# Optimization experiments

Hardware: AMD Instinct MI355X
Metric: run time of the kernel (lower is better)

Reference implementation:

```python
import jax, jax.numpy as jnp
import numpy as np

N_NODES = 50000
N_EDGES = 1600000
N_FEAT = 256
HIDDEN = 32
N_CLASS = 64
PROP_RANGE = 4
ALPHA = 0.5
BETA = 1.0


def _spmm(edge_src, edge_dst, edge_val, X):
    # sparse propMatrix @ X : gather source rows, scale by edge weight, scatter-add to dst
    msgs = X[edge_src] * edge_val[:, None]            # [E, C]
    return jax.ops.segment_sum(msgs, edge_dst, num_segments=N_NODES)  # [N, C]


def setup_inputs() -> dict:
    key = jax.random.key(0)
    ks = jax.random.split(key, 8)
    x = jax.random.normal(ks[0], (N_NODES, N_FEAT), dtype=jnp.float32)
    edge_src = jax.random.randint(ks[1], (N_EDGES,), 0, N_NODES, dtype=jnp.int32)
    edge_dst = jax.random.randint(ks[2], (N_EDGES,), 0, N_NODES, dtype=jnp.int32)
    edge_val = jax.random.uniform(ks[3], (N_EDGES,), dtype=jnp.float32)
    # predSeq params: Linear(nFeature,32) -> ReLU -> Linear(32,nClass)
    W1 = jax.random.normal(ks[4], (N_FEAT, HIDDEN), dtype=jnp.float32) / np.sqrt(N_FEAT)
    b1 = jnp.zeros((HIDDEN,), dtype=jnp.float32)
    W2 = jax.random.normal(ks[5], (HIDDEN, N_CLASS), dtype=jnp.float32) / np.sqrt(HIDDEN)
    b2 = jnp.zeros((N_CLASS,), dtype=jnp.float32)
    return {"x": x, "edge_src": edge_src, "edge_dst": edge_dst, "edge_val": edge_val,
            "W1": W1, "b1": b1, "W2": W2, "b2": b2}


def reference(x, edge_src, edge_dst, edge_val, W1, b1, W2, b2):
    # predSeq + softmax -> initial pseudo labels [N, nClass]
    h = jax.nn.relu(x @ W1 + b1)
    p = jax.nn.softmax(h @ W2 + b2, axis=1)
    # prop(), mode='none': propRange steps of nonlinear SpMM (dropout = identity in eval)
    for _ in range(PROP_RANGE):
        p = ALPHA * jnp.tanh(BETA * _spmm(edge_src, edge_dst, edge_val, p))
    return jax.nn.softmax(p, axis=1)
```

## Files before the change

kernel.cpp:

```cpp
#include <hip/hip_runtime.h>
#include <hip/hip_bf16.h>
#include <math.h>

#define N_NODES 50000
#define N_EDGES 1600000
#define N_FEAT  256
#define HIDDEN  32
#define N_CLASS 64
#define NBUCK   391
#define EPB     2560
#define BINB    625
#define MLPB    782
#define SCAP    5120
#define CAP     4608

typedef _Float16 half_t;
typedef _Float16 half8 __attribute__((ext_vector_type(8)));

__device__ __forceinline__ float half_tanh(float x) {
  float e = __expf(2.f * x);
  return 0.5f - __builtin_amdgcn_rcpf(e + 1.f);
}


__global__ __launch_bounds__(256) void prep_kernel(
    const float* __restrict__ x, const float* __restrict__ W1,
    const float* __restrict__ b1, const float* __restrict__ W2,
    const float* __restrict__ b2, half_t* __restrict__ P,
    const int* __restrict__ esrc, const int* __restrict__ edst,
    const float* __restrict__ evl, int* __restrict__ bcur,
    int2* __restrict__ st) {
  __shared__ __align__(16) int smem[6684];
  int t = threadIdx.x;

  if (blockIdx.x < MLPB) {
    float* fs = (float*)smem;
    float* xs = fs;
    float* ps = fs;
    float* hfull = fs + 4416;
    int w = __builtin_amdgcn_readfirstlane(t >> 6);
    int l = t & 63;
    int n0 = blockIdx.x * 64;
    int rowb = t >> 4, c4 = t & 15;
    int f0 = c4 * 4;

    float4 v[4];
#pragma unroll
    for (int p = 0; p < 4; ++p) {
      int row = rowb + 16 * p;
      v[p] = make_float4(0.f, 0.f, 0.f, 0.f);
      if (n0 + row < N_NODES)
        v[p] = *(const float4*)(x + (size_t)(n0 + row) * N_FEAT + f0);
    }

    float h[8];
#pragma unroll
    for (int j = 0; j < 8; ++j) h[j] = 0.f;

    for (int kc = 0; kc < 4; ++kc) {
#pragma unroll
      for (int p = 0; p < 4; ++p) {
        int row = rowb + 16 * p;
        int col = (row + f0) & 63;
        xs[(f0 + 0) * 64 + col] = v[p].x;
        xs[(f0 + 1) * 64 + col] = v[p].y;
        xs[(f0 + 2) * 64 + col] = v[p].z;
        xs[(f0 + 3) * 64 + col] = v[p].w;
      }
      __syncthreads();
      if (kc < 3) {
#pragma unroll
        for (int p = 0; p < 4; ++p) {
          int row = rowb + 16 * p;
          v[p] = make_float4(0.f, 0.f, 0.f, 0.f);
          if (n0 + row < N_NODES)
            v[p] = *(const float4*)(x + (size_t)(n0 + row) * N_FEAT + (kc + 1) * 64 + f0);
        }
      }
#pragma unroll 8
      for (int k = 0; k < 64; ++k) {
        float xk = xs[k * 64 + ((l + (k & 60)) & 63)];
        const float* wr = W1 + (size_t)(kc * 64 + k) * HIDDEN + 8 * w;
#pragma unroll
        for (int j = 0; j < 8; ++j) h[j] = fmaf(xk, wr[j], h[j]);
      }
      __syncthreads();
    }

#pragma unroll
    for (int i = 0; i < 8; ++i)
      hfull[l * 33 + 8 * w + i] = fmaxf(h[i] + b1[8 * w + i], 0.f);
    __syncthreads();

    float pa[16];
#pragma unroll
    for (int c = 0; c < 16; ++c) pa[c] = b2[16 * w + c];
#pragma unroll 4
    for (int kk = 0; kk < 32; ++kk) {
      float hk = hfull[l * 33 + kk];
      const float* w2r = W2 + kk * N_CLASS + 16 * w;
#pragma unroll
      for (int c = 0; c < 16; ++c) pa[c] = fmaf(hk, w2r[c], pa[c]);
    }
#pragma unroll
    for (int c = 0; c < 16; ++c) ps[l * 65 + 16 * w + c] = pa[c];
    __syncthreads();

    {
      int n = t >> 2, ck = (t & 3) * 16;
      float q[16];
      float m = -1e30f;
#pragma unroll
      for (int i = 0; i < 16; ++i) { q[i] = ps[n * 65 + ck + i]; m = fmaxf(m, q[i]); }
      m = fmaxf(m, __shfl_xor(m, 1));
      m = fmaxf(m, __shfl_xor(m, 2));
      float s = 0.f;
#pragma unroll
      for (int i = 0; i < 16; ++i) { q[i] = __expf(q[i] - m); s += q[i]; }
      s += __shfl_xor(s, 1);
      s += __shfl_xor(s, 2);
      float inv = 1.f / s;
      if (n0 + n < N_NODES) {
        half8 o0, o1;
#pragma unroll
        for (int i = 0; i < 8; ++i) {
          o0[i] = (half_t)(q[i] * inv);
          o1[i] = (half_t)(q[8 + i] * inv);
        }
        half_t* op = P + (size_t)(n0 + n) * N_CLASS + ck;
        *(half8*)op = o0;
        *(half8*)(op + 8) = o1;
      }
    }
  } else {
    int2* stage = (int2*)smem;
    int* h      = smem + 5120;
    int* lstart = smem + 5511;
    int* lcur   = smem + 5902;
    int* gbase  = smem + 6293;
    int bb = blockIdx.x - MLPB;
    for (int i = t; i < NBUCK; i += 256) { h[i] = 0; lcur[i] = 0; }
    __syncthreads();
    int base = bb * EPB;
    int nloc = min(EPB, N_EDGES - base);
    for (int i = t; i < nloc; i += 256) atomicAdd(&h[edst[base + i] >> 7], 1);
    __syncthreads();
    if (t < 64) {
      int loc[7];
      int s0 = 0;
#pragma unroll
      for (int i = 0; i < 7; ++i) {
        int b = t * 7 + i;
        int c = (b < NBUCK) ? h[b] : 0;
        loc[i] = s0; s0 += c;
      }
      int run = s0;
#pragma unroll
      for (int off = 1; off < 64; off <<= 1) {
        int u = __shfl_up(run, off);
        if (t >= off) run += u;
      }
      int excl = run - s0;
#pragma unroll
      for (int i = 0; i < 7; ++i) {
        int b = t * 7 + i;
        if (b < NBUCK) lstart[b] = excl + loc[i];
      }
    }
    __syncthreads();
    for (int i = t; i < NBUCK; i += 256) {
      int c = h[i];
      gbase[i] = c ? atomicAdd(&bcur[i], c) : 0;
    }
    __syncthreads();
    for (int i = t; i < nloc; i += 256) {
      int e = base + i;
      int d = edst[e];
      int b = d >> 7;
      int pos = lstart[b] + atomicAdd(&lcur[b], 1);
      stage[pos] = make_int2((d << 16) | esrc[e], __float_as_int(evl[e]));
    }
    __syncthreads();
    for (int i = t; i < nloc; i += 256) {
      int2 vv = stage[i];
      int b = (int)(((unsigned)vv.x) >> 23);
      int pos = gbase[b] + (i - lstart[b]);
      if (pos < SCAP) st[(size_t)b * SCAP + pos] = vv;
    }
  }
}


__global__ __launch_bounds__(1024) void build_csr(const int* __restrict__ bcur,
                                                  const int2* __restrict__ st,
                                                  int2* __restrict__ rr,
                                                  int2* __restrict__ ep) {
  __shared__ int2 stage[CAP];
  __shared__ int lh[128], lstart[128], lcur[128];
  int b = blockIdx.x, t = threadIdx.x;
  int n = min(min(bcur[b], SCAP), CAP);
  int gb = b * SCAP;
  if (t < 128) { lh[t] = 0; lcur[t] = 0; }
  __syncthreads();
  for (int i = t; i < n; i += 1024) {
    int2 v = st[gb + i];
    stage[i] = v;
    atomicAdd(&lh[(v.x >> 16) & 127], 1);
  }
  __syncthreads();
  if (t < 64) {
    int a0 = lh[2 * t], a1 = lh[2 * t + 1];
    int s0 = a0 + a1;
    int run = s0;
#pragma unroll
    for (int off = 1; off < 64; off <<= 1) {
      int u = __shfl_up(run, off);
      if (t >= off) run += u;
    }
    int excl = run - s0;
    lstart[2 * t] = excl;
    lstart[2 * t + 1] = excl + a0;
  }
  __syncthreads();
  int nodebase = b * 128;
  int nn = min(128, N_NODES - nodebase);
  if (t < nn)
    rr[nodebase + t] = make_int2(gb + lstart[t], gb + lstart[t] + lh[t]);
  for (int i = t; i < n; i += 1024) {
    int2 v = stage[i];
    int d = (v.x >> 16) & 127;
    int pos = lstart[d] + atomicAdd(&lcur[d], 1);
    ep[gb + pos] = make_int2(v.x & 0xffff, v.y);
  }
}


template <int FINAL>
__global__ __launch_bounds__(256) void spmm_kernel(const int2* __restrict__ rr,
                                                   const long long* __restrict__ epl,
                                                   const half_t* __restrict__ pin,
                                                   void* __restrict__ pout_) {
  int node = blockIdx.x * 4 + (threadIdx.x >> 6);
  int lane = threadIdx.x & 63;
  int g = lane >> 3;
  int s = lane & 7;
  int2 be = rr[node];
  int beg = be.x, end = be.y;
  int deg = end - beg;
  float acc[8];
#pragma unroll
  for (int i = 0; i < 8; ++i) acc[i] = 0.f;
  if (deg <= 64) {
    int idx = beg + lane;
    long long raw = (lane < deg) ? epl[idx] : 0LL;
    int ex = (int)raw;
    float ev = __int_as_float((int)(raw >> 32));
#pragma unroll 4
    for (int j = g; j < deg; j += 8) {
      int   sj = __shfl(ex, j);
      float vj = __shfl(ev, j);
      half8 hv = *(const half8*)(pin + ((size_t)sj << 6) + (s << 3));
#pragma unroll
      for (int i = 0; i < 8; ++i) acc[i] = fmaf(vj, (float)hv[i], acc[i]);
    }
  } else {
    for (int base = beg; base < end; base += 64) {
      int idx = base + lane;
      long long raw = (idx < end) ? epl[idx] : 0LL;
      int ex = (int)raw;
      float ev = __int_as_float((int)(raw >> 32));
      int cnt = min(64, end - base);
#pragma unroll 4
      for (int j = g; j < cnt; j += 8) {
        int   sj = __shfl(ex, j);
        float vj = __shfl(ev, j);
        half8 hv = *(const half8*)(pin + ((size_t)sj << 6) + (s << 3));
#pragma unroll
        for (int i = 0; i < 8; ++i) acc[i] = fmaf(vj, (float)hv[i], acc[i]);
      }
    }
  }
#pragma unroll
  for (int off = 8; off <= 32; off <<= 1)
#pragma unroll
    for (int i = 0; i < 8; ++i) acc[i] += __shfl_xor(acc[i], off);
  float r[8];
#pragma unroll
  for (int i = 0; i < 8; ++i) r[i] = half_tanh(acc[i]);
  if (FINAL) {
    float m = r[0];
#pragma unroll
    for (int i = 1; i < 8; ++i) m = fmaxf(m, r[i]);
    m = fmaxf(m, __shfl_xor(m, 1));
    m = fmaxf(m, __shfl_xor(m, 2));
    m = fmaxf(m, __shfl_xor(m, 4));
    float e[8], sum = 0.f;
#pragma unroll
    for (int i = 0; i < 8; ++i) { e[i] = __expf(r[i] - m); sum += e[i]; }
    sum += __shfl_xor(sum, 1);
    sum += __shfl_xor(sum, 2);
    sum += __shfl_xor(sum, 4);
    float inv = 1.f / sum;
    if (g == 0) {
      float* op = (float*)pout_ + ((size_t)node << 6) + (s << 3);
      *(float4*)op = make_float4(e[0] * inv, e[1] * inv, e[2] * inv, e[3] * inv);
      *(float4*)(op + 4) = make_float4(e[4] * inv, e[5] * inv, e[6] * inv, e[7] * inv);
    }
  } else {
    if (g == 0) {
      half8 o;
#pragma unroll
      for (int i = 0; i < 8; ++i) o[i] = (half_t)r[i];
      *(half8*)((half_t*)pout_ + ((size_t)node << 6) + (s << 3)) = o;
    }
  }
}


extern "C" void kernel_launch(void* const* d_in, const int* in_sizes, int n_in,
                              void* d_out, int out_size, void* d_ws, size_t ws_size,
                              hipStream_t stream) {
  const float* x    = (const float*)d_in[0];
  const int*   esrc = (const int*)d_in[1];
  const int*   edst = (const int*)d_in[2];
  const float* evl  = (const float*)d_in[3];
  const float* W1   = (const float*)d_in[4];
  const float* b1   = (const float*)d_in[5];
  const float* W2   = (const float*)d_in[6];
  const float* b2   = (const float*)d_in[7];

  char* ws = (char*)d_ws;
  int2*   st   = (int2*)  (ws);
  half_t* Pb   = (half_t*)(ws);
  int2*   ep   = (int2*)  (ws + 16015360);
  half_t* Pa   = (half_t*)(ws + 32030720);
  int*    bcur = (int*)   (ws + 38430720);
  int2*   rr   = (int2*)  (ws + 38432320);

  hipMemsetAsync(bcur, 0, NBUCK * sizeof(int), stream);

  prep_kernel<<<MLPB + BINB, 256, 0, stream>>>(x, W1, b1, W2, b2, Pa,
                                               esrc, edst, evl, bcur, st);
  build_csr<<<NBUCK, 1024, 0, stream>>>(bcur, st, rr, ep);

  const long long* epl = (const long long*)ep;
  spmm_kernel<0><<<12500, 256, 0, stream>>>(rr, epl, Pa, (void*)Pb);
  spmm_kernel<0><<<12500, 256, 0, stream>>>(rr, epl, Pb, (void*)Pa);
  spmm_kernel<0><<<12500, 256, 0, stream>>>(rr, epl, Pa, (void*)Pb);
  spmm_kernel<1><<<12500, 256, 0, stream>>>(rr, epl, Pb, d_out);
}
```

Baseline: 267.1 us.

## Fuse CSR build and four SpMM steps into one persistent kernel

Merges build_csr and the four spmm launches into a single kernel of 391 blocks of 1024 threads. Each block keeps its bucket's sorted edge list in shared memory and processes its own 128 destination nodes across all steps, with a hand-written global atomic barrier between steps. This removes launch gaps, the global CSR write, and the edge-list re-reads. In exchange, the SpMM work runs on only 391 blocks (one wave per node), so there is less parallelism and latency hiding. The spin barrier also relies on all blocks being resident at the same time.

```diff
diff --git a/kernel.cpp b/kernel.cpp
--- a/kernel.cpp
+++ b/kernel.cpp
@@ -191,10 +191,28 @@
 }
 
 
-__global__ __launch_bounds__(1024) void build_csr(const int* __restrict__ bcur,
-                                                  const int2* __restrict__ st,
-                                                  int2* __restrict__ rr,
-                                                  int2* __restrict__ ep) {
+__device__ __forceinline__ void gsync(unsigned* __restrict__ bar, int phase) {
+  __syncthreads();
+  if (threadIdx.x == 0) {
+    __threadfence();
+    unsigned old = atomicAdd(&bar[phase], 1u);
+    if (old == NBUCK - 1) {
+      __hip_atomic_store(&bar[4 + phase], 1u, __ATOMIC_RELEASE,
+                         __HIP_MEMORY_SCOPE_AGENT);
+    } else {
+      while (__hip_atomic_load(&bar[4 + phase], __ATOMIC_ACQUIRE,
+                               __HIP_MEMORY_SCOPE_AGENT) == 0)
+        __builtin_amdgcn_s_sleep(8);
+    }
+    __threadfence();
+  }
+  __syncthreads();
+}
+
+__global__ __launch_bounds__(1024, 4) void mega_spmm(
+    const int* __restrict__ bcur, const int2* __restrict__ st,
+    half_t* __restrict__ Pa, half_t* __restrict__ Pb,
+    float* __restrict__ outp, unsigned* __restrict__ bar) {
   __shared__ int2 stage[CAP];
   __shared__ int lh[128], lstart[128], lcur[128];
   int b = blockIdx.x, t = threadIdx.x;
@@ -203,9 +221,9 @@
   if (t < 128) { lh[t] = 0; lcur[t] = 0; }
   __syncthreads();
   for (int i = t; i < n; i += 1024) {
-    int2 v = st[gb + i];
-    stage[i] = v;
-    atomicAdd(&lh[(v.x >> 16) & 127], 1);
+    int2 e = st[gb + i];
+    stage[i] = e;
+    atomicAdd(&lh[(e.x >> 16) & 127], 1);
   }
   __syncthreads();
   if (t < 64) {
@@ -222,97 +240,78 @@
     lstart[2 * t + 1] = excl + a0;
   }
   __syncthreads();
-  int nodebase = b * 128;
-  int nn = min(128, N_NODES - nodebase);
-  if (t < nn)
-    rr[nodebase + t] = make_int2(gb + lstart[t], gb + lstart[t] + lh[t]);
+  int2 v[5]; int pos[5]; int np = 0;
   for (int i = t; i < n; i += 1024) {
-    int2 v = stage[i];
-    int d = (v.x >> 16) & 127;
-    int pos = lstart[d] + atomicAdd(&lcur[d], 1);
-    ep[gb + pos] = make_int2(v.x & 0xffff, v.y);
-  }
-}
-
-
-template <int FINAL>
-__global__ __launch_bounds__(256) void spmm_kernel(const int2* __restrict__ rr,
-                                                   const long long* __restrict__ epl,
-                                                   const half_t* __restrict__ pin,
-                                                   void* __restrict__ pout_) {
-  int node = blockIdx.x * 4 + (threadIdx.x >> 6);
-  int lane = threadIdx.x & 63;
+    int2 e = stage[i];
+    int d = (e.x >> 16) & 127;
+    v[np] = e;
+    pos[np] = lstart[d] + atomicAdd(&lcur[d], 1);
+    ++np;
+  }
+  __syncthreads();
+  for (int k = 0; k < np; ++k) stage[pos[k]] = v[k];
+  __syncthreads();
+
+  int w = t >> 6;
+  int lane = t & 63;
   int g = lane >> 3;
   int s = lane & 7;
-  int2 be = rr[node];
-  int beg = be.x, end = be.y;
-  int deg = end - beg;
-  float acc[8];
-#pragma unroll
-  for (int i = 0; i < 8; ++i) acc[i] = 0.f;
-  if (deg <= 64) {
-    int idx = beg + lane;
-    long long raw = (lane < deg) ? epl[idx] : 0LL;
-    int ex = (int)raw;
-    float ev = __int_as_float((int)(raw >> 32));
+  for (int r = 0; r < 4; ++r) {
+    const half_t* pin = (r & 1) ? Pb : Pa;
+    half_t* pout = (r & 1) ? Pa : Pb;
+#pragma unroll 1
+    for (int ni = 0; ni < 8; ++ni) {
+      int d = w * 8 + ni;
+      int deg = lh[d], base = lstart[d];
+      int node = b * 128 + d;
+      float acc[8];
+#pragma unroll
+      for (int i = 0; i < 8; ++i) acc[i] = 0.f;
 #pragma unroll 4
-    for (int j = g; j < deg; j += 8) {
-      int   sj = __shfl(ex, j);
-      float vj = __shfl(ev, j);
-      half8 hv = *(const half8*)(pin + ((size_t)sj << 6) + (s << 3));
-#pragma unroll
-      for (int i = 0; i < 8; ++i) acc[i] = fmaf(vj, (float)hv[i], acc[i]);
-    }
-  } else {
-    for (int base = beg; base < end; base += 64) {
-      int idx = base + lane;
-      long long raw = (idx < end) ? epl[idx] : 0LL;
-      int ex = (int)raw;
-      float ev = __int_as_float((int)(raw >> 32));
-      int cnt = min(64, end - base);
-#pragma unroll 4
-      for (int j = g; j < cnt; j += 8) {
-        int   sj = __shfl(ex, j);
-        float vj = __shfl(ev, j);
-        half8 hv = *(const half8*)(pin + ((size_t)sj << 6) + (s << 3));
+      for (int j = g; j < deg; j += 8) {
+        int2 e = stage[base + j];
+        float vj = __int_as_float(e.y);
+        int src = e.x & 0xffff;
+        half8 hv = *(const half8*)(pin + ((size_t)src << 6) + (s << 3));
 #pragma unroll
         for (int i = 0; i < 8; ++i) acc[i] = fmaf(vj, (float)hv[i], acc[i]);
       }
-    }
-  }
-#pragma unroll
-  for (int off = 8; off <= 32; off <<= 1)
-#pragma unroll
-    for (int i = 0; i < 8; ++i) acc[i] += __shfl_xor(acc[i], off);
-  float r[8];
-#pragma unroll
-  for (int i = 0; i < 8; ++i) r[i] = half_tanh(acc[i]);
-  if (FINAL) {
-    float m = r[0];
-#pragma unroll
-    for (int i = 1; i < 8; ++i) m = fmaxf(m, r[i]);
-    m = fmaxf(m, __shfl_xor(m, 1));
-    m = fmaxf(m, __shfl_xor(m, 2));
-    m = fmaxf(m, __shfl_xor(m, 4));
-    float e[8], sum = 0.f;
-#pragma unroll
-    for (int i = 0; i < 8; ++i) { e[i] = __expf(r[i] - m); sum += e[i]; }
-    sum += __shfl_xor(sum, 1);
-    sum += __shfl_xor(sum, 2);
-    sum += __shfl_xor(sum, 4);
-    float inv = 1.f / sum;
-    if (g == 0) {
-      float* op = (float*)pout_ + ((size_t)node << 6) + (s << 3);
-      *(float4*)op = make_float4(e[0] * inv, e[1] * inv, e[2] * inv, e[3] * inv);
-      *(float4*)(op + 4) = make_float4(e[4] * inv, e[5] * inv, e[6] * inv, e[7] * inv);
-    }
-  } else {
-    if (g == 0) {
-      half8 o;
-#pragma unroll
-      for (int i = 0; i < 8; ++i) o[i] = (half_t)r[i];
-      *(half8*)((half_t*)pout_ + ((size_t)node << 6) + (s << 3)) = o;
-    }
+#pragma unroll
+      for (int off = 8; off <= 32; off <<= 1)
+#pragma unroll
+        for (int i = 0; i < 8; ++i) acc[i] += __shfl_xor(acc[i], off);
+      float rv[8];
+#pragma unroll
+      for (int i = 0; i < 8; ++i) rv[i] = half_tanh(acc[i]);
+      if (r < 3) {
+        if (g == 0 && node < N_NODES) {
+          half8 o;
+#pragma unroll
+          for (int i = 0; i < 8; ++i) o[i] = (half_t)rv[i];
+          *(half8*)(pout + ((size_t)node << 6) + (s << 3)) = o;
+        }
+      } else {
+        float m = rv[0];
+#pragma unroll
+        for (int i = 1; i < 8; ++i) m = fmaxf(m, rv[i]);
+        m = fmaxf(m, __shfl_xor(m, 1));
+        m = fmaxf(m, __shfl_xor(m, 2));
+        m = fmaxf(m, __shfl_xor(m, 4));
+        float e[8], sum = 0.f;
+#pragma unroll
+        for (int i = 0; i < 8; ++i) { e[i] = __expf(rv[i] - m); sum += e[i]; }
+        sum += __shfl_xor(sum, 1);
+        sum += __shfl_xor(sum, 2);
+        sum += __shfl_xor(sum, 4);
+        float inv = 1.f / sum;
+        if (g == 0 && node < N_NODES) {
+          float* op = outp + ((size_t)node << 6) + (s << 3);
+          *(float4*)op = make_float4(e[0] * inv, e[1] * inv, e[2] * inv, e[3] * inv);
+          *(float4*)(op + 4) = make_float4(e[4] * inv, e[5] * inv, e[6] * inv, e[7] * inv);
+        }
+      }
+    }
+    if (r < 3) gsync(bar, r);
   }
 }
 
@@ -330,22 +329,15 @@
   const float* b2   = (const float*)d_in[7];
 
   char* ws = (char*)d_ws;
-  int2*   st   = (int2*)  (ws);
-  half_t* Pb   = (half_t*)(ws);
-  int2*   ep   = (int2*)  (ws + 16015360);
-  half_t* Pa   = (half_t*)(ws + 32030720);
-  int*    bcur = (int*)   (ws + 38430720);
-  int2*   rr   = (int2*)  (ws + 38432320);
-
-  hipMemsetAsync(bcur, 0, NBUCK * sizeof(int), stream);
+  int2*     st   = (int2*)    (ws);
+  half_t*   Pa   = (half_t*)  (ws + 16015360);
+  half_t*   Pb   = (half_t*)  (ws + 22415360);
+  int*      bcur = (int*)     (ws + 28815360);
+  unsigned* bar  = (unsigned*)(ws + 28816960);
+
+  hipMemsetAsync(ws + 28815360, 0, 1632, stream);
 
   prep_kernel<<<MLPB + BINB, 256, 0, stream>>>(x, W1, b1, W2, b2, Pa,
                                                esrc, edst, evl, bcur, st);
-  build_csr<<<NBUCK, 1024, 0, stream>>>(bcur, st, rr, ep);
-
-  const long long* epl = (const long long*)ep;
-  spmm_kernel<0><<<12500, 256, 0, stream>>>(rr, epl, Pa, (void*)Pb);
-  spmm_kernel<0><<<12500, 256, 0, stream>>>(rr, epl, Pb, (void*)Pa);
-  spmm_kernel<0><<<12500, 256, 0, stream>>>(rr, epl, Pa, (void*)Pb);
-  spmm_kernel<1><<<12500, 256, 0, stream>>>(rr, epl, Pb, d_out);
-}
+  mega_spmm<<<NBUCK, 1024, 0, stream>>>(bcur, st, Pa, Pb, (float*)d_out, bar);
+}
```

After: 528.5 us. 97.9% more time.

## Split propagation feature matrix into two 32-column halves for cache locality

Applied to the files above, without the earlier changes.

Stores the fp16 label matrix as two separate 32-column planes (lo/hi) and runs the three intermediate SpMM steps as a kernel whose blocks each handle one half for a node group. The blocks are interleaved so that each XCD group works on one half. This shrinks the working set each gather touches, aiming for better L2/MALL hit rates on the random source-row reads. Edge list loads become nontemporal. The cost is that every edge list is read twice, once per half, and the blocks are smaller.

```diff
diff --git a/kernel.cpp b/kernel.cpp
--- a/kernel.cpp
+++ b/kernel.cpp
@@ -13,6 +13,7 @@
 #define MLPB    782
 #define SCAP    5120
 #define CAP     4608
+#define SPLITB  25000
 
 typedef _Float16 half_t;
 typedef _Float16 half8 __attribute__((ext_vector_type(8)));
@@ -26,7 +27,8 @@
 __global__ __launch_bounds__(256) void prep_kernel(
     const float* __restrict__ x, const float* __restrict__ W1,
     const float* __restrict__ b1, const float* __restrict__ W2,
-    const float* __restrict__ b2, half_t* __restrict__ P,
+    const float* __restrict__ b2, half_t* __restrict__ Plo,
+    half_t* __restrict__ Phi,
     const int* __restrict__ esrc, const int* __restrict__ edst,
     const float* __restrict__ evl, int* __restrict__ bcur,
     int2* __restrict__ st) {
@@ -127,7 +129,9 @@
           o0[i] = (half_t)(q[i] * inv);
           o1[i] = (half_t)(q[8 + i] * inv);
         }
-        half_t* op = P + (size_t)(n0 + n) * N_CLASS + ck;
+        half_t* op = (ck < 32)
+            ? Plo + (size_t)(n0 + n) * 32 + ck
+            : Phi + (size_t)(n0 + n) * 32 + (ck - 32);
         *(half8*)op = o0;
         *(half8*)(op + 8) = o1;
       }
@@ -235,15 +239,80 @@
 }
 
 
-template <int FINAL>
-__global__ __launch_bounds__(256) void spmm_kernel(const int2* __restrict__ rr,
-                                                   const long long* __restrict__ epl,
-                                                   const half_t* __restrict__ pin,
-                                                   void* __restrict__ pout_) {
+__global__ __launch_bounds__(256) void spmm_half(const int2* __restrict__ rr,
+                                                 const long long* __restrict__ epl,
+                                                 const half_t* __restrict__ plo,
+                                                 const half_t* __restrict__ phi,
+                                                 half_t* __restrict__ qlo,
+                                                 half_t* __restrict__ qhi) {
+  int bid = blockIdx.x;
+  int xc = bid & 7;
+  int hf = xc >> 2;
+  int ng = (bid >> 3) * 4 + (xc & 3);
+  int node = ng * 4 + (threadIdx.x >> 6);
+  int lane = threadIdx.x & 63;
+  int g = lane >> 2;
+  int s = lane & 3;
+  const half_t* pin = hf ? phi : plo;
+  half_t* pout = hf ? qhi : qlo;
+  int2 be = rr[node];
+  int beg = be.x, end = be.y;
+  int deg = end - beg;
+  float acc[8];
+#pragma unroll
+  for (int i = 0; i < 8; ++i) acc[i] = 0.f;
+  if (deg <= 64) {
+    long long raw = (lane < deg) ? __builtin_nontemporal_load(epl + beg + lane) : 0LL;
+    int ex = (int)raw;
+    float ev = __int_as_float((int)(raw >> 32));
+#pragma unroll 4
+    for (int j = g; j < deg; j += 16) {
+      int   sj = __shfl(ex, j);
+      float vj = __shfl(ev, j);
+      half8 hv = *(const half8*)(pin + ((size_t)sj << 5) + (s << 3));
+#pragma unroll
+      for (int i = 0; i < 8; ++i) acc[i] = fmaf(vj, (float)hv[i], acc[i]);
+    }
+  } else {
+    for (int base = beg; base < end; base += 64) {
+      int idx = base + lane;
+      long long raw = (idx < end) ? __builtin_nontemporal_load(epl + idx) : 0LL;
+      int ex = (int)raw;
+      float ev = __int_as_float((int)(raw >> 32));
+      int cnt = min(64, end - base);
+#pragma unroll 4
+      for (int j = g; j < cnt; j += 16) {
+        int   sj = __shfl(ex, j);
+        float vj = __shfl(ev, j);
+        half8 hv = *(const half8*)(pin + ((size_t)sj << 5) + (s << 3));
+#pragma unroll
+        for (int i = 0; i < 8; ++i) acc[i] = fmaf(vj, (float)hv[i], acc[i]);
+      }
+    }
+  }
+#pragma unroll
+  for (int off = 4; off <= 32; off <<= 1)
+#pragma unroll
+    for (int i = 0; i < 8; ++i) acc[i] += __shfl_xor(acc[i], off);
+  if (g == 0) {
+    half8 o;
+#pragma unroll
+    for (int i = 0; i < 8; ++i) o[i] = (half_t)half_tanh(acc[i]);
+    *(half8*)(pout + ((size_t)node << 5) + (s << 3)) = o;
+  }
+}
+
+
+__global__ __launch_bounds__(256) void spmm_final(const int2* __restrict__ rr,
+                                                  const long long* __restrict__ epl,
+                                                  const half_t* __restrict__ plo,
+                                                  const half_t* __restrict__ phi,
+                                                  float* __restrict__ outp) {
   int node = blockIdx.x * 4 + (threadIdx.x >> 6);
   int lane = threadIdx.x & 63;
   int g = lane >> 3;
   int s = lane & 7;
+  const half_t* gb = (s < 4) ? (plo + ((size_t)s << 3)) : (phi + ((size_t)(s - 4) << 3));
   int2 be = rr[node];
   int beg = be.x, end = be.y;
   int deg = end - beg;
@@ -251,22 +320,21 @@
 #pragma unroll
   for (int i = 0; i < 8; ++i) acc[i] = 0.f;
   if (deg <= 64) {
-    int idx = beg + lane;
-    long long raw = (lane < deg) ? epl[idx] : 0LL;
+    long long raw = (lane < deg) ? __builtin_nontemporal_load(epl + beg + lane) : 0LL;
     int ex = (int)raw;
     float ev = __int_as_float((int)(raw >> 32));
 #pragma unroll 4
     for (int j = g; j < deg; j += 8) {
       int   sj = __shfl(ex, j);
       float vj = __shfl(ev, j);
-      half8 hv = *(const half8*)(pin + ((size_t)sj << 6) + (s << 3));
+      half8 hv = *(const half8*)(gb + ((size_t)sj << 5));
 #pragma unroll
       for (int i = 0; i < 8; ++i) acc[i] = fmaf(vj, (float)hv[i], acc[i]);
     }
   } else {
     for (int base = beg; base < end; base += 64) {
       int idx = base + lane;
-      long long raw = (idx < end) ? epl[idx] : 0LL;
+      long long raw = (idx < end) ? __builtin_nontemporal_load(epl + idx) : 0LL;
       int ex = (int)raw;
       float ev = __int_as_float((int)(raw >> 32));
       int cnt = min(64, end - base);
@@ -274,7 +342,7 @@
       for (int j = g; j < cnt; j += 8) {
         int   sj = __shfl(ex, j);
         float vj = __shfl(ev, j);
-        half8 hv = *(const half8*)(pin + ((size_t)sj << 6) + (s << 3));
+        half8 hv = *(const half8*)(gb + ((size_t)sj << 5));
 #pragma unroll
         for (int i = 0; i < 8; ++i) acc[i] = fmaf(vj, (float)hv[i], acc[i]);
       }
@@ -287,32 +355,23 @@
   float r[8];
 #pragma unroll
   for (int i = 0; i < 8; ++i) r[i] = half_tanh(acc[i]);
-  if (FINAL) {
-    float m = r[0];
-#pragma unroll
-    for (int i = 1; i < 8; ++i) m = fmaxf(m, r[i]);
-    m = fmaxf(m, __shfl_xor(m, 1));
-    m = fmaxf(m, __shfl_xor(m, 2));
-    m = fmaxf(m, __shfl_xor(m, 4));
-    float e[8], sum = 0.f;
-#pragma unroll
-    for (int i = 0; i < 8; ++i) { e[i] = __expf(r[i] - m); sum += e[i]; }
-    sum += __shfl_xor(sum, 1);
-    sum += __shfl_xor(sum, 2);
-    sum += __shfl_xor(sum, 4);
-    float inv = 1.f / sum;
-    if (g == 0) {
-      float* op = (float*)pout_ + ((size_t)node << 6) + (s << 3);
-      *(float4*)op = make_float4(e[0] * inv, e[1] * inv, e[2] * inv, e[3] * inv);
-      *(float4*)(op + 4) = make_float4(e[4] * inv, e[5] * inv, e[6] * inv, e[7] * inv);
-    }
-  } else {
-    if (g == 0) {
-      half8 o;
-#pragma unroll
-      for (int i = 0; i < 8; ++i) o[i] = (half_t)r[i];
-      *(half8*)((half_t*)pout_ + ((size_t)node << 6) + (s << 3)) = o;
-    }
+  float m = r[0];
+#pragma unroll
+  for (int i = 1; i < 8; ++i) m = fmaxf(m, r[i]);
+  m = fmaxf(m, __shfl_xor(m, 1));
+  m = fmaxf(m, __shfl_xor(m, 2));
+  m = fmaxf(m, __shfl_xor(m, 4));
+  float e[8], sum = 0.f;
+#pragma unroll
+  for (int i = 0; i < 8; ++i) { e[i] = __expf(r[i] - m); sum += e[i]; }
+  sum += __shfl_xor(sum, 1);
+  sum += __shfl_xor(sum, 2);
+  sum += __shfl_xor(sum, 4);
+  float inv = 1.f / sum;
+  if (g == 0) {
+    float* op = outp + ((size_t)node << 6) + (s << 3);
+    *(float4*)op = make_float4(e[0] * inv, e[1] * inv, e[2] * inv, e[3] * inv);
+    *(float4*)(op + 4) = make_float4(e[4] * inv, e[5] * inv, e[6] * inv, e[7] * inv);
   }
 }
 
@@ -330,22 +389,24 @@
   const float* b2   = (const float*)d_in[7];
 
   char* ws = (char*)d_ws;
-  int2*   st   = (int2*)  (ws);
-  half_t* Pb   = (half_t*)(ws);
-  int2*   ep   = (int2*)  (ws + 16015360);
-  half_t* Pa   = (half_t*)(ws + 32030720);
-  int*    bcur = (int*)   (ws + 38430720);
-  int2*   rr   = (int2*)  (ws + 38432320);
+  int2*   st    = (int2*)  (ws);
+  half_t* PbLo  = (half_t*)(ws);
+  half_t* PbHi  = (half_t*)(ws + 3200000);
+  int2*   ep    = (int2*)  (ws + 16015360);
+  half_t* PaLo  = (half_t*)(ws + 32030720);
+  half_t* PaHi  = (half_t*)(ws + 35230720);
+  int*    bcur  = (int*)   (ws + 38430720);
+  int2*   rr    = (int2*)  (ws + 38432320);
 
   hipMemsetAsync(bcur, 0, NBUCK * sizeof(int), stream);
 
-  prep_kernel<<<MLPB + BINB, 256, 0, stream>>>(x, W1, b1, W2, b2, Pa,
+  prep_kernel<<<MLPB + BINB, 256, 0, stream>>>(x, W1, b1, W2, b2, PaLo, PaHi,
                                                esrc, edst, evl, bcur, st);
   build_csr<<<NBUCK, 1024, 0, stream>>>(bcur, st, rr, ep);
 
   const long long* epl = (const long long*)ep;
-  spmm_kernel<0><<<12500, 256, 0, stream>>>(rr, epl, Pa, (void*)Pb);
-  spmm_kernel<0><<<12500, 256, 0, stream>>>(rr, epl, Pb, (void*)Pa);
-  spmm_kernel<0><<<12500, 256, 0, stream>>>(rr, epl, Pa, (void*)Pb);
-  spmm_kernel<1><<<12500, 256, 0, stream>>>(rr, epl, Pb, d_out);
-}
+  spmm_half<<<SPLITB, 256, 0, stream>>>(rr, epl, PaLo, PaHi, PbLo, PbHi);
+  spmm_half<<<SPLITB, 256, 0, stream>>>(rr, epl, PbLo, PbHi, PaLo, PaHi);
+  spmm_half<<<SPLITB, 256, 0, stream>>>(rr, epl, PaLo, PaHi, PbLo, PbHi);
+  spmm_final<<<12500, 256, 0, stream>>>(rr, epl, PbLo, PbHi, (float*)d_out);
+}
```

New measurement: 329.3 us. 23.3% more time.

## Process two nodes per wavefront in SpMM and run binning blocks first in prep

Applied to the files above, without the earlier changes.

The SpMM kernel now assigns each half-wavefront of 32 lanes to one destination node, so a 256-thread block handles 8 nodes and the grid is halved. Edges are fetched in chunks of 32 with 4 edge groups per half, and the final reduction needs fewer shuffle steps. This targets idle lanes, since the average degree is about 32 and a full 64-lane wave per node left many lanes unused. Separately, the prep kernel puts the edge-binning blocks at the lowest block indices so they are scheduled before the MLP blocks. The per-node gather parallelism drops, which may raise latency for high-degree nodes.

```diff
diff --git a/kernel.cpp b/kernel.cpp
--- a/kernel.cpp
+++ b/kernel.cpp
@@ -33,14 +33,14 @@
   __shared__ __align__(16) int smem[6684];
   int t = threadIdx.x;
 
-  if (blockIdx.x < MLPB) {
+  if (blockIdx.x >= BINB) {
     float* fs = (float*)smem;
     float* xs = fs;
     float* ps = fs;
     float* hfull = fs + 4416;
     int w = __builtin_amdgcn_readfirstlane(t >> 6);
     int l = t & 63;
-    int n0 = blockIdx.x * 64;
+    int n0 = (blockIdx.x - BINB) * 64;
     int rowb = t >> 4, c4 = t & 15;
     int f0 = c4 * 4;
 
@@ -138,7 +138,7 @@
     int* lstart = smem + 5511;
     int* lcur   = smem + 5902;
     int* gbase  = smem + 6293;
-    int bb = blockIdx.x - MLPB;
+    int bb = blockIdx.x;
     for (int i = t; i < NBUCK; i += 256) { h[i] = 0; lcur[i] = 0; }
     __syncthreads();
     int base = bb * EPB;
@@ -240,48 +240,36 @@
                                                    const long long* __restrict__ epl,
                                                    const half_t* __restrict__ pin,
                                                    void* __restrict__ pout_) {
-  int node = blockIdx.x * 4 + (threadIdx.x >> 6);
-  int lane = threadIdx.x & 63;
-  int g = lane >> 3;
+  int tid = threadIdx.x;
+  int lane = tid & 63;
+  int hf = lane >> 5;
+  int sl = lane & 31;
+  int g = sl >> 3;
   int s = lane & 7;
+  int node = blockIdx.x * 8 + (tid >> 6) * 2 + hf;
   int2 be = rr[node];
   int beg = be.x, end = be.y;
-  int deg = end - beg;
   float acc[8];
 #pragma unroll
   for (int i = 0; i < 8; ++i) acc[i] = 0.f;
-  if (deg <= 64) {
-    int idx = beg + lane;
-    long long raw = (lane < deg) ? epl[idx] : 0LL;
+  for (int base = beg; base < end; base += 32) {
+    int idx = base + sl;
+    long long raw = (idx < end) ? epl[idx] : 0LL;
     int ex = (int)raw;
     float ev = __int_as_float((int)(raw >> 32));
+    int cnt = min(32, end - base);
 #pragma unroll 4
-    for (int j = g; j < deg; j += 8) {
-      int   sj = __shfl(ex, j);
-      float vj = __shfl(ev, j);
+    for (int j = g; j < cnt; j += 4) {
+      int srcl = (hf << 5) + j;
+      int   sj = __shfl(ex, srcl);
+      float vj = __shfl(ev, srcl);
       half8 hv = *(const half8*)(pin + ((size_t)sj << 6) + (s << 3));
 #pragma unroll
       for (int i = 0; i < 8; ++i) acc[i] = fmaf(vj, (float)hv[i], acc[i]);
     }
-  } else {
-    for (int base = beg; base < end; base += 64) {
-      int idx = base + lane;
-      long long raw = (idx < end) ? epl[idx] : 0LL;
-      int ex = (int)raw;
-      float ev = __int_as_float((int)(raw >> 32));
-      int cnt = min(64, end - base);
-#pragma unroll 4
-      for (int j = g; j < cnt; j += 8) {
-        int   sj = __shfl(ex, j);
-        float vj = __shfl(ev, j);
-        half8 hv = *(const half8*)(pin + ((size_t)sj << 6) + (s << 3));
-#pragma unroll
-        for (int i = 0; i < 8; ++i) acc[i] = fmaf(vj, (float)hv[i], acc[i]);
-      }
-    }
-  }
-#pragma unroll
-  for (int off = 8; off <= 32; off <<= 1)
+  }
+#pragma unroll
+  for (int off = 8; off <= 16; off <<= 1)
 #pragma unroll
     for (int i = 0; i < 8; ++i) acc[i] += __shfl_xor(acc[i], off);
   float r[8];
@@ -344,8 +332,8 @@
   build_csr<<<NBUCK, 1024, 0, stream>>>(bcur, st, rr, ep);
 
   const long long* epl = (const long long*)ep;
-  spmm_kernel<0><<<12500, 256, 0, stream>>>(rr, epl, Pa, (void*)Pb);
-  spmm_kernel<0><<<12500, 256, 0, stream>>>(rr, epl, Pb, (void*)Pa);
-  spmm_kernel<0><<<12500, 256, 0, stream>>>(rr, epl, Pa, (void*)Pb);
-  spmm_kernel<1><<<12500, 256, 0, stream>>>(rr, epl, Pb, d_out);
-}
+  spmm_kernel<0><<<6250, 256, 0, stream>>>(rr, epl, Pa, (void*)Pb);
+  spmm_kernel<0><<<6250, 256, 0, stream>>>(rr, epl, Pb, (void*)Pa);
+  spmm_kernel<0><<<6250, 256, 0, stream>>>(rr, epl, Pa, (void*)Pb);
+  spmm_kernel<1><<<6250, 256, 0, stream>>>(rr, epl, Pb, d_out);
+}
```

Result: faster. 260.2 us (-2.6%).
